# Optimization experiments

Measured on AMD Instinct MI355X. Metric: run time of the kernel, lower is better.

The kernel has to match this reference:

```python
import jax, jax.numpy as jnp
import numpy as np

B, H, W, C = 16, 64, 64, 384
DH = 32                 # dim_head
NH = C // DH            # heads = dim // dim_head
WS = 8                  # window_size
DFF = 4 * C             # dim_ff default = 4*dim
EPS = 1e-5


def setup_inputs() -> dict:
    key = jax.random.key(0)
    ks = jax.random.split(key, 6)
    rn = lambda k, shape, scale: (jax.random.normal(k, shape, jnp.float32) * scale)
    return {
        "x": rn(ks[0], (B, H, W, C), 1.0),
        "w_qkv": rn(ks[1], (C, 3 * NH * DH), 0.02),   # fused qkv projection, bias=False
        "w_out": rn(ks[2], (NH * DH, C), 0.02),       # attention output projection
        "gamma_attn": jnp.ones((C,), jnp.float32),     # LayerNormNoBias2d weight (post-attn)
        "w1": rn(ks[3], (C, DFF), 0.02),               # FFN up projection
        "w2": rn(ks[4], (DFF, C), 0.02),               # FFN down projection
        "gamma_ff": jnp.ones((C,), jnp.float32),       # LayerNormNoBias2d weight (post-FFN)
    }


def _shift2d(x):
    # S2-MLP style 4-way spatial shift of channel quarters, zero-filled at borders.
    c4 = x.shape[-1] // 4
    g1 = jnp.pad(x[:, :-1, :, 0 * c4:1 * c4], ((0, 0), (1, 0), (0, 0), (0, 0)))  # shift down
    g2 = jnp.pad(x[:, 1:, :, 1 * c4:2 * c4], ((0, 0), (0, 1), (0, 0), (0, 0)))   # shift up
    g3 = jnp.pad(x[:, :, :-1, 2 * c4:3 * c4], ((0, 0), (0, 0), (1, 0), (0, 0)))  # shift right
    g4 = jnp.pad(x[:, :, 1:, 3 * c4:4 * c4], ((0, 0), (0, 0), (0, 1), (0, 0)))   # shift left
    return jnp.concatenate([g1, g2, g3, g4], axis=-1)


def _ln_nobias(x, gamma):
    # LayerNorm over channel dim, weight only (no bias).
    mu = jnp.mean(x, axis=-1, keepdims=True)
    var = jnp.var(x, axis=-1, keepdims=True)
    return (x - mu) * jax.lax.rsqrt(var + EPS) * gamma


def _window_attention(x, w_qkv, w_out):
    # Grouped (non-overlapping) window multi-head self-attention.
    b, h, w, c = x.shape
    nh, nw = h // WS, w // WS
    T = WS * WS
    # partition into windows: (b*nh*nw, T, c)
    xw = x.reshape(b, nh, WS, nw, WS, c).transpose(0, 1, 3, 2, 4, 5).reshape(b * nh * nw, T, c)
    qkv = xw @ w_qkv                                   # (n, T, 3*NH*DH)
    qkv = qkv.reshape(-1, T, 3, NH, DH)
    q = qkv[:, :, 0].transpose(0, 2, 1, 3)             # (n, NH, T, DH)
    k = qkv[:, :, 1].transpose(0, 2, 1, 3)
    v = qkv[:, :, 2].transpose(0, 2, 1, 3)
    logits = jnp.einsum('nhqd,nhkd->nhqk', q, k) * (DH ** -0.5)
    attn = jax.nn.softmax(logits, axis=-1)
    o = jnp.einsum('nhqk,nhkd->nhqd', attn, v)         # (n, NH, T, DH)
    o = o.transpose(0, 2, 1, 3).reshape(-1, T, NH * DH) @ w_out
    # un-window back to (b, h, w, c)
    return o.reshape(b, nh, nw, WS, WS, c).transpose(0, 1, 3, 2, 4, 5).reshape(b, h, w, c)


def reference(x, w_qkv, w_out, gamma_attn, w1, w2, gamma_ff):
    # x = x + DropBlock(Norm(GWAttn(Shift2d(x))))   (drop rates = 0 -> identity)
    a = _window_attention(_shift2d(x), w_qkv, w_out)
    x = x + _ln_nobias(a, gamma_attn)
    # x = x + DropBlock(Norm(FF(x)))
    f = jax.nn.gelu(x @ w1, approximate=False) @ w2
    return x + _ln_nobias(f, gamma_ff)
```

## Files before the change

kernel.cpp:

```cpp
#include <hip/hip_runtime.h>
#include <hip/hip_bf16.h>
#include <math.h>

typedef __attribute__((ext_vector_type(8))) __bf16 bf16x8;
typedef __attribute__((ext_vector_type(4))) float f32x4;
typedef unsigned int uint32;

static constexpr int kC   = 384;
static constexpr int kNH  = 12;
static constexpr int kDH  = 32;
static constexpr int kT   = 64;
static constexpr int kH   = 64;
static constexpr int kW   = 64;
static constexpr int kDFF = 1536;
static constexpr long kNTOK = 65536;
static constexpr long kNT  = kNTOK * kC;

__device__ __forceinline__ float bf_lo(uint32 u){ return __uint_as_float(u << 16); }
__device__ __forceinline__ float bf_hi(uint32 u){ return __uint_as_float(u & 0xffff0000u); }

__device__ __forceinline__ float gelu_fast(float x) {
    float x2 = x * x;
    float t  = fmaf(0.102944787f, x2, 2.302208165f);
    float m  = fminf(x * t, 80.0f);
    float e  = __builtin_amdgcn_exp2f(m);
    float d  = 1.0f + e;
    return x * e * __builtin_amdgcn_rcpf(d);
}

__global__ void k_transpose_cast(const float* __restrict__ src, __bf16* __restrict__ dst,
                                 int K, int N)
{
    int o = blockIdx.x * 256 + threadIdx.x;
    if (o >= K * N) return;
    int n = o / K, k = o - n * K;
    dst[o] = (__bf16)src[(size_t)k * N + n];
}

__global__ __launch_bounds__(256) void k_shift_window(const float* __restrict__ x,
                                                      __bf16* __restrict__ Aw)
{
    int tid = blockIdx.x * 256 + threadIdx.x;
    int m = tid / 48;
    int g = tid - m * 48;
    int c0 = g * 8;
    int wi = m >> 6, t = m & 63;
    int b = wi >> 6, nh = (wi >> 3) & 7, nw = wi & 7;
    int h = nh * 8 + (t >> 3);
    int w = nw * 8 + (t & 7);
    int q = c0 / 96;
    int sh = h, sw = w;
    bool ok;
    if      (q == 0) { sh = h - 1; ok = (h >= 1);  }
    else if (q == 1) { sh = h + 1; ok = (h <= 62); }
    else if (q == 2) { sw = w - 1; ok = (w >= 1);  }
    else             { sw = w + 1; ok = (w <= 62); }

    __bf16 r[8] __attribute__((aligned(16)));
    if (ok) {
        const float4* src = reinterpret_cast<const float4*>(
            x + (((size_t)b * kH + sh) * kW + sw) * kC + c0);
        float4 v0 = src[0], v1 = src[1];
        r[0] = (__bf16)v0.x; r[1] = (__bf16)v0.y; r[2] = (__bf16)v0.z; r[3] = (__bf16)v0.w;
        r[4] = (__bf16)v1.x; r[5] = (__bf16)v1.y; r[6] = (__bf16)v1.z; r[7] = (__bf16)v1.w;
    } else {
        #pragma unroll
        for (int i = 0; i < 8; ++i) r[i] = (__bf16)0.0f;
    }
    *reinterpret_cast<int4*>(Aw + (size_t)m * kC + c0) = *reinterpret_cast<int4*>(r);
}

template<int EPI>
__global__ __launch_bounds__(512) void k_gemm(const __bf16* __restrict__ A,
                                              const __bf16* __restrict__ B,
                                              __bf16* __restrict__ Cout,
                                              int N, int K, int nt)
{
    __shared__ __align__(16) __bf16 As[3][256 * 32];
    __shared__ __align__(16) __bf16 Bs[2][128 * 32];
    const int tid  = threadIdx.x;
    const int wave = tid >> 6, lane = tid & 63;
    const int g = lane >> 4, qh = lane & 15;

    const int nwg = gridDim.x;
    const int wg  = (blockIdx.x & 7) * (nwg >> 3) + (blockIdx.x >> 3);
    const int nb  = wg % nt, mb = wg / nt;
    const int m0 = mb * 256, n0 = nb * 128;
    const int wr = (wave >> 1) * 64;
    const int wc = (wave & 1) * 64;

    const int sw = ((g ^ ((lane >> 1) & 3)) << 3);

    auto STAGE_A = [&](int buf, int t) {
        const int k0 = t << 5;
        #pragma unroll
        for (int i = 0; i < 2; ++i) {
            int idx = tid + i * 512;
            int row = idx >> 2;
            int gseg = (idx & 3) ^ ((idx >> 3) & 3);
            __builtin_amdgcn_global_load_lds(
                (const __attribute__((address_space(1))) void*)(A + (size_t)(m0 + row) * K + k0 + gseg * 8),
                (__attribute__((address_space(3))) void*)(&As[buf][idx * 8]), 16, 0, 0);
        }
    };
    auto STAGE_B = [&](int buf, int t) {
        const int k0 = t << 5;
        int idx = tid;
        int row = idx >> 2;
        int gseg = (idx & 3) ^ ((idx >> 3) & 3);
        __builtin_amdgcn_global_load_lds(
            (const __attribute__((address_space(1))) void*)(B + (size_t)(n0 + row) * K + k0 + gseg * 8),
            (__attribute__((address_space(3))) void*)(&Bs[buf][idx * 8]), 16, 0, 0);
    };

    f32x4 acc[4][4] = {};
    const int nkt = K >> 5;

    STAGE_A(0, 0);
    __builtin_amdgcn_sched_barrier(0);
    STAGE_B(0, 0);
    __builtin_amdgcn_sched_barrier(0);
    STAGE_A(1, 1);
    __builtin_amdgcn_sched_barrier(0);

    int ca = 0, sa = 2;
    for (int t = 0; t < nkt; ++t) {
        if (t + 1 < nkt) asm volatile("s_waitcnt vmcnt(2)" ::: "memory");
        else             asm volatile("s_waitcnt vmcnt(0)" ::: "memory");
        __builtin_amdgcn_s_barrier();
        __builtin_amdgcn_sched_barrier(0);
        if (t + 1 < nkt) STAGE_B((t + 1) & 1, t + 1);
        __builtin_amdgcn_sched_barrier(0);
        if (t + 2 < nkt) STAGE_A(sa, t + 2);
        __builtin_amdgcn_sched_barrier(0);

        bf16x8 af[4], bfr[4];
        #pragma unroll
        for (int mi = 0; mi < 4; ++mi) {
            int ra = wr + mi * 16 + qh;
            af[mi] = *reinterpret_cast<const bf16x8*>(&As[ca][ra * 32 + sw]);
        }
        #pragma unroll
        for (int ni = 0; ni < 4; ++ni) {
            int rb = wc + ni * 16 + qh;
            bfr[ni] = *reinterpret_cast<const bf16x8*>(&Bs[t & 1][rb * 32 + sw]);
        }
        __builtin_amdgcn_s_setprio(1);
        #pragma unroll
        for (int mi = 0; mi < 4; ++mi)
            #pragma unroll
            for (int ni = 0; ni < 4; ++ni)
                acc[mi][ni] = __builtin_amdgcn_mfma_f32_16x16x32_bf16(bfr[ni], af[mi], acc[mi][ni], 0, 0, 0);
        __builtin_amdgcn_s_setprio(0);

        ca = (ca == 2) ? 0 : ca + 1;
        sa = (sa == 2) ? 0 : sa + 1;
    }

    #pragma unroll
    for (int mi = 0; mi < 4; ++mi) {
        const int row = m0 + wr + mi * 16 + qh;
        size_t rowoff = 0;
        if constexpr (EPI == 0) {
            rowoff = (((size_t)(row >> 6)) * kNH * 64 + (row & 63)) * kDH;
        }
        #pragma unroll
        for (int ni = 0; ni < 4; ++ni) {
            const int nb4 = n0 + wc + ni * 16 + (g << 2);
            __bf16 tmp[4] __attribute__((aligned(8)));
            #pragma unroll
            for (int r = 0; r < 4; ++r) {
                float v = acc[mi][ni][r];
                if constexpr (EPI == 2) v = gelu_fast(v);
                tmp[r] = (__bf16)v;
            }
            if constexpr (EPI == 0) {
                int s = nb4 / 384, rem = nb4 - s * 384;
                int hh = rem >> 5, d = rem & 31;
                __bf16* dst = Cout + (size_t)s * kNT + ((size_t)hh * 64) * kDH + rowoff + d;
                *reinterpret_cast<uint2*>(dst) = *reinterpret_cast<const uint2*>(tmp);
            } else {
                *reinterpret_cast<uint2*>(Cout + (size_t)row * N + nb4) =
                    *reinterpret_cast<const uint2*>(tmp);
            }
        }
    }
}

__global__ __launch_bounds__(256) void k_attn(const __bf16* __restrict__ qkv,
                                              __bf16* __restrict__ AO)
{
    __shared__ __bf16 Pl[4][kT * kT];
    const int wave = threadIdx.x >> 6, lane = threadIdx.x & 63;
    const int pair = blockIdx.x * 4 + wave;
    const int wi = pair / kNH, hh = pair - wi * kNH;
    const int g = lane >> 4, qh = lane & 15;

    const __bf16* Qp = qkv + ((size_t)wi * kNH + hh) * (kT * kDH);
    const __bf16* Kp = Qp + kNT;
    const __bf16* Vp = Qp + 2 * kNT;
    char* Pb = (char*)&Pl[wave][0];

    bf16x8 qa[4], kb[4];
    #pragma unroll
    for (int mi = 0; mi < 4; ++mi)
        qa[mi] = *reinterpret_cast<const bf16x8*>(Qp + (mi * 16 + qh) * kDH + g * 8);
    #pragma unroll
    for (int ni = 0; ni < 4; ++ni)
        kb[ni] = *reinterpret_cast<const bf16x8*>(Kp + (ni * 16 + qh) * kDH + g * 8);

    f32x4 s[4][4] = {};
    #pragma unroll
    for (int mi = 0; mi < 4; ++mi)
        #pragma unroll
        for (int ni = 0; ni < 4; ++ni)
            s[mi][ni] = __builtin_amdgcn_mfma_f32_16x16x32_bf16(qa[mi], kb[ni], s[mi][ni], 0, 0, 0);

    const float scale = 0.17677669529663687f;
    float rmax[4][4], rsum[4][4];
    #pragma unroll
    for (int mi = 0; mi < 4; ++mi)
        #pragma unroll
        for (int r = 0; r < 4; ++r) {
            float a = fmaxf(fmaxf(s[mi][0][r], s[mi][1][r]), fmaxf(s[mi][2][r], s[mi][3][r]));
            #pragma unroll
            for (int st = 1; st < 16; st <<= 1) a = fmaxf(a, __shfl_xor(a, st));
            rmax[mi][r] = a;
        }
    #pragma unroll
    for (int mi = 0; mi < 4; ++mi)
        #pragma unroll
        for (int r = 0; r < 4; ++r) {
            float acc = 0.f;
            #pragma unroll
            for (int ni = 0; ni < 4; ++ni) {
                float p = __expf((s[mi][ni][r] - rmax[mi][r]) * scale);
                s[mi][ni][r] = p;
                acc += p;
            }
            #pragma unroll
            for (int st = 1; st < 16; st <<= 1) acc += __shfl_xor(acc, st);
            rsum[mi][r] = 1.0f / acc;
        }

    #pragma unroll
    for (int mi = 0; mi < 4; ++mi)
        #pragma unroll
        for (int ni = 0; ni < 4; ++ni)
            #pragma unroll
            for (int r = 0; r < 4; ++r) {
                int row = mi * 16 + g * 4 + r;
                int col = ni * 16 + qh;
                uint32 byte = (uint32)((row << 7) | (col << 1)) ^ (uint32)((row & 7) << 4);
                *reinterpret_cast<__bf16*>(Pb + byte) = (__bf16)s[mi][ni][r];
            }

    f32x4 o[4][2] = {};
    #pragma unroll
    for (int kk = 0; kk < 2; ++kk) {
        bf16x8 pa[4], vb[2];
        #pragma unroll
        for (int mi = 0; mi < 4; ++mi) {
            int row = mi * 16 + qh;
            uint32 byte = (uint32)((row << 7) | (kk << 6) | (g << 4)) ^ (uint32)((row & 7) << 4);
            pa[mi] = *reinterpret_cast<const bf16x8*>(Pb + byte);
        }
        #pragma unroll
        for (int n2 = 0; n2 < 2; ++n2) {
            __bf16 tmp[8];
            #pragma unroll
            for (int j = 0; j < 8; ++j)
                tmp[j] = Vp[(kk * 32 + g * 8 + j) * kDH + n2 * 16 + qh];
            vb[n2] = *reinterpret_cast<const bf16x8*>(tmp);
        }
        #pragma unroll
        for (int mi = 0; mi < 4; ++mi)
            #pragma unroll
            for (int n2 = 0; n2 < 2; ++n2)
                o[mi][n2] = __builtin_amdgcn_mfma_f32_16x16x32_bf16(pa[mi], vb[n2], o[mi][n2], 0, 0, 0);
    }

    #pragma unroll
    for (int mi = 0; mi < 4; ++mi)
        #pragma unroll
        for (int n2 = 0; n2 < 2; ++n2)
            #pragma unroll
            for (int r = 0; r < 4; ++r) {
                int row = mi * 16 + g * 4 + r;
                AO[((size_t)wi * 64 + row) * kC + hh * kDH + n2 * 16 + qh] =
                    (__bf16)(o[mi][n2][r] * rsum[mi][r]);
            }
}

__global__ __launch_bounds__(256) void k_ln_res1(const __bf16* __restrict__ P,
                                                 const float* __restrict__ x,
                                                 const float* __restrict__ gamma,
                                                 __bf16* __restrict__ X1)
{
    const int wave = threadIdx.x >> 6, lane = threadIdx.x & 63;
    const int tok = blockIdx.x * 4 + wave;
    const int b = tok >> 12, hw = tok & 4095, h = hw >> 6, w = hw & 63;
    const int m = (((b << 6) | ((h >> 3) << 3) | (w >> 3)) << 6) | (((h & 7) << 3) | (w & 7));

    float p[6]; float sum = 0.f, sq = 0.f;
    #pragma unroll
    for (int i = 0; i < 6; ++i) {
        p[i] = (float)P[(size_t)m * kC + lane + i * 64];
        sum += p[i]; sq += p[i] * p[i];
    }
    #pragma unroll
    for (int off = 32; off; off >>= 1) { sum += __shfl_xor(sum, off); sq += __shfl_xor(sq, off); }
    float mean = sum * (1.0f / kC);
    float var  = sq * (1.0f / kC) - mean * mean;
    float rs   = rsqrtf(var + 1e-5f);
    #pragma unroll
    for (int i = 0; i < 6; ++i) {
        int c = lane + i * 64;
        float v = x[(size_t)tok * kC + c] + (p[i] - mean) * rs * gamma[c];
        X1[(size_t)tok * kC + c] = (__bf16)v;
    }
}

__global__ __launch_bounds__(256) void k_ln_res2(const __bf16* __restrict__ F,
                                                 const __bf16* __restrict__ X1,
                                                 const float* __restrict__ gamma,
                                                 float* __restrict__ out)
{
    const int wave = threadIdx.x >> 6, lane = threadIdx.x & 63;
    const size_t tok = blockIdx.x * 4 + wave;

    float f[6]; float sum = 0.f, sq = 0.f;
    #pragma unroll
    for (int i = 0; i < 6; ++i) {
        f[i] = (float)F[tok * kC + lane + i * 64];
        sum += f[i]; sq += f[i] * f[i];
    }
    #pragma unroll
    for (int off = 32; off; off >>= 1) { sum += __shfl_xor(sum, off); sq += __shfl_xor(sq, off); }
    float mean = sum * (1.0f / kC);
    float var  = sq * (1.0f / kC) - mean * mean;
    float rs   = rsqrtf(var + 1e-5f);
    #pragma unroll
    for (int i = 0; i < 6; ++i) {
        int c = lane + i * 64;
        out[tok * kC + c] = (float)X1[tok * kC + c] + (f[i] - mean) * rs * gamma[c];
    }
}

extern "C" void kernel_launch(void* const* d_in, const int* in_sizes, int n_in,
                              void* d_out, int out_size, void* d_ws, size_t ws_size,
                              hipStream_t stream) {
    const float* x    = (const float*)d_in[0];
    const float* wqkv = (const float*)d_in[1];
    const float* wout = (const float*)d_in[2];
    const float* g_at = (const float*)d_in[3];
    const float* w1   = (const float*)d_in[4];
    const float* w2   = (const float*)d_in[5];
    const float* g_ff = (const float*)d_in[6];
    float* out = (float*)d_out;

    char* ws = (char*)d_ws;
    size_t off = 0;
    auto alloc = [&](size_t bytes) { size_t o = off; off += (bytes + 255) & ~(size_t)255; return o; };
    __bf16* WqkvT = (__bf16*)(ws + alloc((size_t)1152 * 384 * 2));
    __bf16* WoutT = (__bf16*)(ws + alloc((size_t)384 * 384 * 2));
    __bf16* W1T   = (__bf16*)(ws + alloc((size_t)1536 * 384 * 2));
    __bf16* W2T   = (__bf16*)(ws + alloc((size_t)384 * 1536 * 2));
    __bf16* R1    = (__bf16*)(ws + alloc((size_t)kNTOK * kDFF * 2));
    __bf16* R2    = (__bf16*)(ws + alloc((size_t)kNT * 2));
    __bf16* R3    = (__bf16*)(ws + alloc((size_t)kNT * 2));

    k_transpose_cast<<<dim3((384 * 1152 + 255) / 256), 256, 0, stream>>>(wqkv, WqkvT, 384, 1152);
    k_transpose_cast<<<dim3((384 * 384 + 255) / 256), 256, 0, stream>>>(wout, WoutT, 384, 384);
    k_transpose_cast<<<dim3((384 * 1536 + 255) / 256), 256, 0, stream>>>(w1, W1T, 384, 1536);
    k_transpose_cast<<<dim3((1536 * 384 + 255) / 256), 256, 0, stream>>>(w2, W2T, 1536, 384);

    k_shift_window<<<dim3(12288), 256, 0, stream>>>(x, R2);

    k_gemm<0><<<dim3(256 * 9), 512, 0, stream>>>(R2, WqkvT, R1, 1152, 384, 9);

    k_attn<<<dim3(3072), 256, 0, stream>>>(R1, R2);

    k_gemm<1><<<dim3(256 * 3), 512, 0, stream>>>(R2, WoutT, R3, 384, 384, 3);

    k_ln_res1<<<dim3(16384), 256, 0, stream>>>(R3, x, g_at, R2);

    k_gemm<2><<<dim3(256 * 12), 512, 0, stream>>>(R2, W1T, R1, 1536, 384, 12);

    k_gemm<1><<<dim3(256 * 3), 512, 0, stream>>>(R1, W2T, R3, 384, 1536, 3);

    k_ln_res2<<<dim3(16384), 256, 0, stream>>>(R3, R2, g_ff, out);
}
```

Before: 522.2 us.

## Replace 512-thread 256x128 GEMM tiles with single-wave 64x64 tiles

Restructures the bf16 MFMA GEMM from 8-wave workgroups computing 256x128 tiles into single-wave workgroups computing 64x64 tiles, each with private double-buffered LDS staging. Workgroup barriers go away and the pipeline is rewritten to issue the next stage after the fragment reads finish. The cost is much less operand reuse per LDS byte and higher global/L2 traffic, since each wave loads both A and B tiles alone. The grid grows to many small blocks.

```diff
diff --git a/kernel.cpp b/kernel.cpp
--- a/kernel.cpp
+++ b/kernel.cpp
@@ -71,80 +71,74 @@
 }
 
 template<int EPI>
-__global__ __launch_bounds__(512) void k_gemm(const __bf16* __restrict__ A,
-                                              const __bf16* __restrict__ B,
-                                              __bf16* __restrict__ Cout,
-                                              int N, int K, int nt)
-{
-    __shared__ __align__(16) __bf16 As[3][256 * 32];
-    __shared__ __align__(16) __bf16 Bs[2][128 * 32];
-    const int tid  = threadIdx.x;
-    const int wave = tid >> 6, lane = tid & 63;
+__global__ __launch_bounds__(64) void k_gemm(const __bf16* __restrict__ A,
+                                             const __bf16* __restrict__ B,
+                                             __bf16* __restrict__ Cout,
+                                             int N, int K, int nt)
+{
+    __shared__ __align__(16) __bf16 Asw[2][64 * 32];
+    __shared__ __align__(16) __bf16 Bsw[2][64 * 32];
+    const int lane = threadIdx.x;
     const int g = lane >> 4, qh = lane & 15;
 
     const int nwg = gridDim.x;
     const int wg  = (blockIdx.x & 7) * (nwg >> 3) + (blockIdx.x >> 3);
     const int nb  = wg % nt, mb = wg / nt;
-    const int m0 = mb * 256, n0 = nb * 128;
-    const int wr = (wave >> 1) * 64;
-    const int wc = (wave & 1) * 64;
+    const int m0 = mb * 64, n0 = nb * 64;
 
     const int sw = ((g ^ ((lane >> 1) & 3)) << 3);
 
-    auto STAGE_A = [&](int buf, int t) {
+    auto STAGE = [&](int buf, int t) {
         const int k0 = t << 5;
         #pragma unroll
-        for (int i = 0; i < 2; ++i) {
-            int idx = tid + i * 512;
+        for (int i = 0; i < 4; ++i) {
+            int idx = lane + i * 64;
             int row = idx >> 2;
             int gseg = (idx & 3) ^ ((idx >> 3) & 3);
             __builtin_amdgcn_global_load_lds(
                 (const __attribute__((address_space(1))) void*)(A + (size_t)(m0 + row) * K + k0 + gseg * 8),
-                (__attribute__((address_space(3))) void*)(&As[buf][idx * 8]), 16, 0, 0);
-        }
-    };
-    auto STAGE_B = [&](int buf, int t) {
-        const int k0 = t << 5;
-        int idx = tid;
-        int row = idx >> 2;
-        int gseg = (idx & 3) ^ ((idx >> 3) & 3);
-        __builtin_amdgcn_global_load_lds(
-            (const __attribute__((address_space(1))) void*)(B + (size_t)(n0 + row) * K + k0 + gseg * 8),
-            (__attribute__((address_space(3))) void*)(&Bs[buf][idx * 8]), 16, 0, 0);
+                (__attribute__((address_space(3))) void*)(&Asw[buf][idx * 8]), 16, 0, 0);
+        }
+        #pragma unroll
+        for (int i = 0; i < 4; ++i) {
+            int idx = lane + i * 64;
+            int row = idx >> 2;
+            int gseg = (idx & 3) ^ ((idx >> 3) & 3);
+            __builtin_amdgcn_global_load_lds(
+                (const __attribute__((address_space(1))) void*)(B + (size_t)(n0 + row) * K + k0 + gseg * 8),
+                (__attribute__((address_space(3))) void*)(&Bsw[buf][idx * 8]), 16, 0, 0);
+        }
     };
 
     f32x4 acc[4][4] = {};
     const int nkt = K >> 5;
 
-    STAGE_A(0, 0);
+    STAGE(0, 0);
     __builtin_amdgcn_sched_barrier(0);
-    STAGE_B(0, 0);
+    STAGE(1, 1);
     __builtin_amdgcn_sched_barrier(0);
-    STAGE_A(1, 1);
-    __builtin_amdgcn_sched_barrier(0);
-
-    int ca = 0, sa = 2;
+
     for (int t = 0; t < nkt; ++t) {
-        if (t + 1 < nkt) asm volatile("s_waitcnt vmcnt(2)" ::: "memory");
+        const int cur = t & 1;
+        if (t + 1 < nkt) asm volatile("s_waitcnt vmcnt(8)" ::: "memory");
         else             asm volatile("s_waitcnt vmcnt(0)" ::: "memory");
-        __builtin_amdgcn_s_barrier();
         __builtin_amdgcn_sched_barrier(0);
-        if (t + 1 < nkt) STAGE_B((t + 1) & 1, t + 1);
-        __builtin_amdgcn_sched_barrier(0);
-        if (t + 2 < nkt) STAGE_A(sa, t + 2);
-        __builtin_amdgcn_sched_barrier(0);
 
         bf16x8 af[4], bfr[4];
         #pragma unroll
-        for (int mi = 0; mi < 4; ++mi) {
-            int ra = wr + mi * 16 + qh;
-            af[mi] = *reinterpret_cast<const bf16x8*>(&As[ca][ra * 32 + sw]);
-        }
-        #pragma unroll
-        for (int ni = 0; ni < 4; ++ni) {
-            int rb = wc + ni * 16 + qh;
-            bfr[ni] = *reinterpret_cast<const bf16x8*>(&Bs[t & 1][rb * 32 + sw]);
-        }
+        for (int mi = 0; mi < 4; ++mi)
+            af[mi] = *reinterpret_cast<const bf16x8*>(&Asw[cur][(mi * 16 + qh) * 32 + sw]);
+        #pragma unroll
+        for (int ni = 0; ni < 4; ++ni)
+            bfr[ni] = *reinterpret_cast<const bf16x8*>(&Bsw[cur][(ni * 16 + qh) * 32 + sw]);
+
+        if (t + 2 < nkt) {
+            asm volatile("s_waitcnt lgkmcnt(0)" ::: "memory");
+            __builtin_amdgcn_sched_barrier(0);
+            STAGE(cur, t + 2);
+            __builtin_amdgcn_sched_barrier(0);
+        }
+
         __builtin_amdgcn_s_setprio(1);
         #pragma unroll
         for (int mi = 0; mi < 4; ++mi)
@@ -152,21 +146,18 @@
             for (int ni = 0; ni < 4; ++ni)
                 acc[mi][ni] = __builtin_amdgcn_mfma_f32_16x16x32_bf16(bfr[ni], af[mi], acc[mi][ni], 0, 0, 0);
         __builtin_amdgcn_s_setprio(0);
-
-        ca = (ca == 2) ? 0 : ca + 1;
-        sa = (sa == 2) ? 0 : sa + 1;
     }
 
     #pragma unroll
     for (int mi = 0; mi < 4; ++mi) {
-        const int row = m0 + wr + mi * 16 + qh;
+        const int row = m0 + mi * 16 + qh;
         size_t rowoff = 0;
         if constexpr (EPI == 0) {
             rowoff = (((size_t)(row >> 6)) * kNH * 64 + (row & 63)) * kDH;
         }
         #pragma unroll
         for (int ni = 0; ni < 4; ++ni) {
-            const int nb4 = n0 + wc + ni * 16 + (g << 2);
+            const int nb4 = n0 + ni * 16 + (g << 2);
             __bf16 tmp[4] __attribute__((aligned(8)));
             #pragma unroll
             for (int r = 0; r < 4; ++r) {
@@ -377,17 +368,17 @@
 
     k_shift_window<<<dim3(12288), 256, 0, stream>>>(x, R2);
 
-    k_gemm<0><<<dim3(256 * 9), 512, 0, stream>>>(R2, WqkvT, R1, 1152, 384, 9);
+    k_gemm<0><<<dim3(1024 * 18), 64, 0, stream>>>(R2, WqkvT, R1, 1152, 384, 18);
 
     k_attn<<<dim3(3072), 256, 0, stream>>>(R1, R2);
 
-    k_gemm<1><<<dim3(256 * 3), 512, 0, stream>>>(R2, WoutT, R3, 384, 384, 3);
+    k_gemm<1><<<dim3(1024 * 6), 64, 0, stream>>>(R2, WoutT, R3, 384, 384, 6);
 
     k_ln_res1<<<dim3(16384), 256, 0, stream>>>(R3, x, g_at, R2);
 
-    k_gemm<2><<<dim3(256 * 12), 512, 0, stream>>>(R2, W1T, R1, 1536, 384, 12);
-
-    k_gemm<1><<<dim3(256 * 3), 512, 0, stream>>>(R1, W2T, R3, 384, 1536, 3);
+    k_gemm<2><<<dim3(1024 * 24), 64, 0, stream>>>(R2, W1T, R1, 1536, 384, 24);
+
+    k_gemm<1><<<dim3(1024 * 6), 64, 0, stream>>>(R1, W2T, R3, 384, 1536, 6);
 
     k_ln_res2<<<dim3(16384), 256, 0, stream>>>(R3, R2, g_ff, out);
 }
```

New measurement: 692.4 us. 1.33x slower.
